# Kernel tuning notes

Measured on AMD Instinct MI355X. Metric: run time of the kernel, lower is better.

Reference implementation:

```python
import jax, jax.numpy as jnp
import numpy as np

B, T, S = 64, 8000, 10


def _linear_sum_assignment(cost):
    """O(n^3) Hungarian (Jonker-Volgenant / e-maxx variant) on a square numpy cost matrix.
    Returns (row_idx, col_idx) minimizing the assignment cost, like scipy."""
    cost = np.asarray(cost, dtype=np.float64)
    n = cost.shape[0]
    u = np.zeros(n + 1)
    v = np.zeros(n + 1)
    p = np.zeros(n + 1, dtype=np.int64)   # p[j] = row (1-based) assigned to column j
    way = np.zeros(n + 1, dtype=np.int64)
    for i in range(1, n + 1):
        p[0] = i
        j0 = 0
        minv = np.full(n + 1, np.inf)
        used = np.zeros(n + 1, dtype=bool)
        while True:
            used[j0] = True
            i0 = p[j0]
            delta = np.inf
            j1 = 0
            for j in range(1, n + 1):
                if not used[j]:
                    cur = cost[i0 - 1, j - 1] - u[i0] - v[j]
                    if cur < minv[j]:
                        minv[j] = cur
                        way[j] = j0
                    if minv[j] < delta:
                        delta = minv[j]
                        j1 = j
            for j in range(n + 1):
                if used[j]:
                    u[p[j]] += delta
                    v[j] -= delta
                else:
                    minv[j] -= delta
            j0 = j1
            if p[j0] == 0:
                break
        while j0:
            j1 = way[j0]
            p[j0] = p[j1]
            j0 = j1
    cols = np.zeros(n, dtype=np.int64)
    for j in range(1, n + 1):
        cols[p[j] - 1] = j - 1
    return np.arange(n), cols


def _pairwise_bce(predictions, targets):
    """pairwise[b, i, j] = mean_t BCE(predictions[b, t, i], targets[b, t, j]).
    Computed as an einsum reduction over T instead of materializing the [B,T,S,S] tensor."""
    t_len = predictions.shape[1]
    logp = jnp.log(predictions)
    log1mp = jnp.log1p(-predictions)
    pos = jnp.einsum('bti,btj->bij', logp, targets)          # sum_t t_j * log p_i
    neg = jnp.einsum('bti,btj->bij', log1mp, 1.0 - targets)  # sum_t (1-t_j) * log(1-p_i)
    return -(pos + neg) / t_len


def setup_inputs() -> dict:
    key = jax.random.key(0)
    kp, kt = jax.random.split(key)
    # sigmoid-like predictions bounded away from {0,1} for BCE stability
    predictions = 0.01 + 0.98 * jax.random.uniform(kp, (B, T, S), dtype=jnp.float32)
    targets = (jax.random.uniform(kt, (B, T, S)) < 0.3).astype(jnp.float32)
    return {"predictions": predictions, "targets": targets}


def reference(predictions, targets):
    pairwise = _pairwise_bce(predictions, targets)            # [B, S, S]
    cost = np.asarray(jax.device_get(pairwise))               # detach + host (as in torch .detach().cpu())
    b, s, _ = cost.shape
    cols = np.stack([_linear_sum_assignment(cost[i])[1] for i in range(b)])  # [B, S]
    rows = jnp.arange(s)
    matched = pairwise[jnp.arange(b)[:, None], rows[None, :], jnp.asarray(cols)]  # [B, S]
    # sum over batch of per-sample means, divided by B  ==  global mean (equal sizes)
    return matched.mean()
```

## Files before the change

kernel.cpp:

```cpp
#include <hip/hip_runtime.h>
#include <hip/hip_bf16.h>

#define B_ 64
#define T_ 8000
#define S_ 10
#define NCHUNK 4
#define PAIRS_PER_CHUNK 1000


__global__ __launch_bounds__(256, 1) void pit_cost_kernel(
    const float* __restrict__ pred, const float* __restrict__ tgt,
    float* __restrict__ partial)
{
    const int b     = blockIdx.y;
    const int chunk = blockIdx.x;
    const int tid   = threadIdx.x;

    float acc[110];
#pragma unroll
    for (int v = 0; v < 110; ++v) acc[v] = 0.0f;

    const size_t baseBT = (size_t)b * (T_ * S_);
    const int p0 = chunk * PAIRS_PER_CHUNK;

#pragma unroll
    for (int it = 0; it < 4; ++it) {
        const int rel = it * 256 + tid;
        if (rel < PAIRS_PER_CHUNK) {
            const int p = p0 + rel;
            const size_t off = baseBT + (size_t)p * (2 * S_);
            const float4* P = reinterpret_cast<const float4*>(pred + off);
            const float4* G = reinterpret_cast<const float4*>(tgt + off);
            alignas(16) float pr[20];
            alignas(16) float tg[20];
#pragma unroll
            for (int k = 0; k < 5; ++k) {
                reinterpret_cast<float4*>(pr)[k] = P[k];
                reinterpret_cast<float4*>(tg)[k] = G[k];
            }
#pragma unroll
            for (int u = 0; u < 2; ++u) {
                float d[10];
#pragma unroll
                for (int i = 0; i < 10; ++i) {
                    const float pv = pr[u * 10 + i];
                    const float lm = __logf(1.0f - pv);
                    d[i] = __logf(pv) - lm;
                    acc[100 + i] += lm;
                }
#pragma unroll
                for (int i = 0; i < 10; ++i) {
#pragma unroll
                    for (int j = 0; j < 10; ++j) {
                        acc[i * 10 + j] += d[i] * tg[u * 10 + j];
                    }
                }
            }
        }
    }

    __shared__ float red[4][112];
    const int wave = tid >> 6;
    const int lane = tid & 63;
#pragma unroll
    for (int v = 0; v < 110; ++v) {
        float x = acc[v];
#pragma unroll
        for (int off = 32; off > 0; off >>= 1) x += __shfl_xor(x, off, 64);
        if (lane == 0) red[wave][v] = x;
    }
    __syncthreads();
    if (tid < 110) {
        const float s = red[0][tid] + red[1][tid] + red[2][tid] + red[3][tid];
        partial[((size_t)b * NCHUNK + chunk) * 112 + tid] = s;
    }
}

__global__ __launch_bounds__(256, 1) void pit_dp_kernel(
    const float* __restrict__ partial, float* __restrict__ ws2)
{
    const int b   = blockIdx.x;
    const int tid = threadIdx.x;

    __shared__ float Ms[100];
    __shared__ float Ds[10];
    __shared__ float cost[100];
    __shared__ float dp[1024];

    if (tid < 110) {
        const float* pb = partial + (size_t)b * NCHUNK * 112;
        float s = pb[tid] + pb[112 + tid] + pb[224 + tid] + pb[336 + tid];
        if (tid < 100) Ms[tid] = s;
        else           Ds[tid - 100] = s;
    }
    __syncthreads();
    if (tid < 100) cost[tid] = -(Ms[tid] + Ds[tid / 10]);
    if (tid == 0) dp[0] = 0.0f;
    __syncthreads();

    for (int k = 1; k <= 10; ++k) {
        for (int m = tid; m < 1024; m += 256) {
            if (__popc(m) == k) {
                float best = 3.0e38f;
#pragma unroll
                for (int j = 0; j < 10; ++j) {
                    if (m & (1 << j)) {
                        const float c = dp[m ^ (1 << j)] + cost[(k - 1) * 10 + j];
                        best = fminf(best, c);
                    }
                }
                dp[m] = best;
            }
        }
        __syncthreads();
    }
    if (tid == 0) ws2[b] = dp[1023];
}

__global__ void pit_final_kernel(const float* __restrict__ ws2,
                                 float* __restrict__ out)
{
    const int lane = threadIdx.x;
    float x = ws2[lane];
#pragma unroll
    for (int off = 32; off > 0; off >>= 1) x += __shfl_xor(x, off, 64);
    if (lane == 0) out[0] = x * (1.0f / ((float)T_ * (float)B_ * (float)S_));
}

extern "C" void kernel_launch(void* const* d_in, const int* in_sizes, int n_in,
                              void* d_out, int out_size, void* d_ws, size_t ws_size,
                              hipStream_t stream)
{
    const float* pred = (const float*)d_in[0];
    const float* tgt  = (const float*)d_in[1];
    float* partial = (float*)d_ws;
    float* ws2     = partial + (size_t)B_ * NCHUNK * 112;
    float* out     = (float*)d_out;

    pit_cost_kernel<<<dim3(NCHUNK, B_), 256, 0, stream>>>(pred, tgt, partial);
    pit_dp_kernel<<<B_, 256, 0, stream>>>(partial, ws2);
    pit_final_kernel<<<1, 64, 0, stream>>>(ws2, out);
}
```

Baseline: 126.9 us.

## Double cost-kernel grid to 8 chunks and fold final reduction into atomics

The cost kernel now splits each batch's time axis into 8 chunks, giving 512 blocks. Each thread handles a single block of 4 time steps with 40-float vector loads, replacing the strided loop over pairs. The separate final-reduction kernel is removed: the DP kernel atomically adds each batch's scaled minimum into the output, which the cost kernel zeroes first. This cuts one launch and raises parallelism, at the cost of nondeterministic float summation order and only 250 of 256 threads active.

```diff
diff --git a/kernel.cpp b/kernel.cpp
--- a/kernel.cpp
+++ b/kernel.cpp
@@ -4,56 +4,52 @@
 #define B_ 64
 #define T_ 8000
 #define S_ 10
-#define NCHUNK 4
-#define PAIRS_PER_CHUNK 1000
+#define NCHUNK 8
+#define TPC 1000
+#define QUADS 250
 
 
 __global__ __launch_bounds__(256, 1) void pit_cost_kernel(
     const float* __restrict__ pred, const float* __restrict__ tgt,
-    float* __restrict__ partial)
+    float* __restrict__ partial, float* __restrict__ out)
 {
     const int b     = blockIdx.y;
     const int chunk = blockIdx.x;
     const int tid   = threadIdx.x;
 
+    if (b == 0 && chunk == 0 && tid == 0) out[0] = 0.0f;
+
     float acc[110];
 #pragma unroll
     for (int v = 0; v < 110; ++v) acc[v] = 0.0f;
 
-    const size_t baseBT = (size_t)b * (T_ * S_);
-    const int p0 = chunk * PAIRS_PER_CHUNK;
+    if (tid < QUADS) {
+        const size_t off = (size_t)b * (T_ * S_) + (size_t)chunk * (TPC * S_)
+                         + (size_t)tid * 40;
+        const float4* P = reinterpret_cast<const float4*>(pred + off);
+        const float4* G = reinterpret_cast<const float4*>(tgt + off);
+        alignas(16) float pr[40];
+        alignas(16) float tg[40];
+#pragma unroll
+        for (int k = 0; k < 10; ++k) reinterpret_cast<float4*>(pr)[k] = P[k];
+#pragma unroll
+        for (int k = 0; k < 10; ++k) reinterpret_cast<float4*>(tg)[k] = G[k];
 
 #pragma unroll
-    for (int it = 0; it < 4; ++it) {
-        const int rel = it * 256 + tid;
-        if (rel < PAIRS_PER_CHUNK) {
-            const int p = p0 + rel;
-            const size_t off = baseBT + (size_t)p * (2 * S_);
-            const float4* P = reinterpret_cast<const float4*>(pred + off);
-            const float4* G = reinterpret_cast<const float4*>(tgt + off);
-            alignas(16) float pr[20];
-            alignas(16) float tg[20];
+        for (int u = 0; u < 4; ++u) {
+            float d[10];
 #pragma unroll
-            for (int k = 0; k < 5; ++k) {
-                reinterpret_cast<float4*>(pr)[k] = P[k];
-                reinterpret_cast<float4*>(tg)[k] = G[k];
+            for (int i = 0; i < 10; ++i) {
+                const float pv = pr[u * 10 + i];
+                const float lm = __logf(1.0f - pv);
+                d[i] = __logf(pv) - lm;
+                acc[100 + i] += lm;
             }
 #pragma unroll
-            for (int u = 0; u < 2; ++u) {
-                float d[10];
+            for (int i = 0; i < 10; ++i) {
 #pragma unroll
-                for (int i = 0; i < 10; ++i) {
-                    const float pv = pr[u * 10 + i];
-                    const float lm = __logf(1.0f - pv);
-                    d[i] = __logf(pv) - lm;
-                    acc[100 + i] += lm;
-                }
-#pragma unroll
-                for (int i = 0; i < 10; ++i) {
-#pragma unroll
-                    for (int j = 0; j < 10; ++j) {
-                        acc[i * 10 + j] += d[i] * tg[u * 10 + j];
-                    }
+                for (int j = 0; j < 10; ++j) {
+                    acc[i * 10 + j] += d[i] * tg[u * 10 + j];
                 }
             }
         }
@@ -77,24 +73,24 @@
 }
 
 __global__ __launch_bounds__(256, 1) void pit_dp_kernel(
-    const float* __restrict__ partial, float* __restrict__ ws2)
+    const float* __restrict__ partial, float* __restrict__ out)
 {
     const int b   = blockIdx.x;
     const int tid = threadIdx.x;
 
-    __shared__ float Ms[100];
-    __shared__ float Ds[10];
+    __shared__ float sum[112];
     __shared__ float cost[100];
     __shared__ float dp[1024];
 
     if (tid < 110) {
         const float* pb = partial + (size_t)b * NCHUNK * 112;
-        float s = pb[tid] + pb[112 + tid] + pb[224 + tid] + pb[336 + tid];
-        if (tid < 100) Ms[tid] = s;
-        else           Ds[tid - 100] = s;
+        float s = 0.0f;
+#pragma unroll
+        for (int c = 0; c < NCHUNK; ++c) s += pb[c * 112 + tid];
+        sum[tid] = s;
     }
     __syncthreads();
-    if (tid < 100) cost[tid] = -(Ms[tid] + Ds[tid / 10]);
+    if (tid < 100) cost[tid] = -(sum[tid] + sum[100 + tid / 10]);
     if (tid == 0) dp[0] = 0.0f;
     __syncthreads();
 
@@ -114,17 +110,9 @@
         }
         __syncthreads();
     }
-    if (tid == 0) ws2[b] = dp[1023];
-}
-
-__global__ void pit_final_kernel(const float* __restrict__ ws2,
-                                 float* __restrict__ out)
-{
-    const int lane = threadIdx.x;
-    float x = ws2[lane];
-#pragma unroll
-    for (int off = 32; off > 0; off >>= 1) x += __shfl_xor(x, off, 64);
-    if (lane == 0) out[0] = x * (1.0f / ((float)T_ * (float)B_ * (float)S_));
+    if (tid == 0) {
+        atomicAdd(out, dp[1023] * (1.0f / ((float)T_ * (float)B_ * (float)S_)));
+    }
 }
 
 extern "C" void kernel_launch(void* const* d_in, const int* in_sizes, int n_in,
@@ -134,10 +122,8 @@
     const float* pred = (const float*)d_in[0];
     const float* tgt  = (const float*)d_in[1];
     float* partial = (float*)d_ws;
-    float* ws2     = partial + (size_t)B_ * NCHUNK * 112;
     float* out     = (float*)d_out;
 
-    pit_cost_kernel<<<dim3(NCHUNK, B_), 256, 0, stream>>>(pred, tgt, partial);
-    pit_dp_kernel<<<B_, 256, 0, stream>>>(partial, ws2);
-    pit_final_kernel<<<1, 64, 0, stream>>>(ws2, out);
+    pit_cost_kernel<<<dim3(NCHUNK, B_), 256, 0, stream>>>(pred, tgt, partial, out);
+    pit_dp_kernel<<<B_, 256, 0, stream>>>(partial, out);
 }
```

Result: faster. 123.0 us (-3.1%).
